# Performance work log

Measured on AMD Instinct MI355X. Metric: run time of the kernel, lower is better.

## Reference

```python
import jax, jax.numpy as jnp
import numpy as np

N, K, FC, FX, E = 16384, 16, 2, 32, 256


def _lin_init(key, fin, fout):
    kw, kb = jax.random.split(key)
    s = 1.0 / np.sqrt(fin)
    W = jax.random.uniform(kw, (fin, fout), jnp.float32, -s, s)
    b = jax.random.uniform(kb, (fout,), jnp.float32, -s, s)
    return W, b


def setup_inputs() -> dict:
    key = jax.random.key(0)
    ks = jax.random.split(key, 13)
    c = jax.random.uniform(ks[0], (N, FC), jnp.float32)
    x = jax.random.normal(ks[1], (N, FX), jnp.float32)
    W_coords, b_coords = _lin_init(ks[2], FC, E)
    W_attri, b_attri = _lin_init(ks[3], FX, E)
    W_g1, b_g1 = _lin_init(ks[4], FC, E)
    W_g2, b_g2 = _lin_init(ks[5], E, E)
    W_g3, b_g3 = _lin_init(ks[6], E, E)
    W_f1, b_f1 = _lin_init(ks[7], FX, E)
    W_f2, b_f2 = _lin_init(ks[8], E, E)
    W_f3, b_f3 = _lin_init(ks[9], E, E)
    W_d1, b_d1 = _lin_init(ks[10], 2 * E, 2 * E)
    W_d2, b_d2 = _lin_init(ks[11], 2 * E, 2)
    return dict(c=c, x=x,
                W_coords=W_coords, b_coords=b_coords,
                W_attri=W_attri, b_attri=b_attri,
                W_g1=W_g1, b_g1=b_g1, W_g2=W_g2, b_g2=b_g2, W_g3=W_g3, b_g3=b_g3,
                W_f1=W_f1, b_f1=b_f1, W_f2=W_f2, b_f2=b_f2, W_f3=W_f3, b_f3=b_f3,
                W_d1=W_d1, b_d1=b_d1, W_d2=W_d2, b_d2=b_d2)


def knn_edges(c, k):
    # PyG knn_graph (loop=False, flow='source_to_target'):
    # edge_index[0]=neighbor(src), edge_index[1]=node(dst).
    n = c.shape[0]
    sq = jnp.sum(c * c, axis=1)
    d2 = sq[:, None] + sq[None, :] - 2.0 * (c @ c.T)  # [N,N] squared dists
    d2 = d2.at[jnp.arange(n), jnp.arange(n)].set(jnp.inf)  # exclude self
    _, idx = jax.lax.top_k(-d2, k)  # [N,k] nearest neighbor indices
    src = idx.reshape(-1)
    dst = jnp.repeat(jnp.arange(n), k)
    return src, dst


def gcn_conv(h, src, dst, ew, W, b):
    # PyG GCNConv: linear -> add self-loops (weight 1) -> sym norm -> scatter-add -> +bias
    n = h.shape[0]
    hw = h @ W
    loop = jnp.arange(n)
    s = jnp.concatenate([src, loop])
    d = jnp.concatenate([dst, loop])
    w = jnp.concatenate([ew, jnp.ones((n,), h.dtype)])
    deg = jax.ops.segment_sum(w, d, num_segments=n)
    dinv = jnp.where(deg > 0, jax.lax.rsqrt(deg), 0.0)
    norm = dinv[s] * w * dinv[d]
    out = jax.ops.segment_sum(norm[:, None] * hw[s], d, num_segments=n)
    return out + b


def reference(c, x, W_coords, b_coords, W_attri, b_attri,
              W_g1, b_g1, W_g2, b_g2, W_g3, b_g3,
              W_f1, b_f1, W_f2, b_f2, W_f3, b_f3,
              W_d1, b_d1, W_d2, b_d2):
    src, dst = knn_edges(c, K)
    dist = jnp.linalg.norm(c[src] - c[dst], axis=1)
    ew = jnp.exp(-dist / 2.0)
    ew = jnp.where(ew > 10.0, 0.0, ew)  # faithful to source (never triggers)

    coords0 = c @ W_coords + b_coords
    attri0 = x @ W_attri + b_attri

    # eval mode: dropout is identity
    g1 = jax.nn.relu(gcn_conv(c, src, dst, ew, W_g1, b_g1))
    m1 = jax.nn.relu(x @ W_f1 + b_f1)
    g1 = coords0 + g1
    m1 = attri0 + m1

    g2 = jax.nn.relu(gcn_conv(g1, src, dst, ew, W_g2, b_g2))
    m2 = jax.nn.relu(m1 @ W_f2 + b_f2)
    g2 = g1 + g2
    m2 = m1 + m2

    g3 = jax.nn.relu(gcn_conv(g2, src, dst, ew, W_g3, b_g3))
    m3 = jax.nn.relu(m2 @ W_f3 + b_f3)
    g3 = g2 + g3
    m3 = m2 + m3

    combined = jnp.concatenate([g3, m3], axis=1)
    out = jax.nn.relu(combined @ W_d1 + b_d1) @ W_d2 + b_d2
    mean = out[:, 0]
    sigma = 0.2 + 0.8 * jax.nn.softplus(out[:, 1])
    return mean.reshape(-1, 1), sigma.reshape(-1, 1), g3, m3
```

## Files before the change

### kernel.cpp

```cpp
#include <hip/hip_runtime.h>
#include <math.h>

#define NPTS 16384
#define KNN 16
#define GRES 128
#define NCELL (GRES * GRES)
#define CAP 16

typedef unsigned long long ull;
typedef __attribute__((ext_vector_type(8))) short  bf16x8;
typedef __attribute__((ext_vector_type(4))) float  f32x4;

__device__ inline unsigned short f2bf(float f) {
    unsigned int u = __float_as_uint(f);
    u += 0x7fffu + ((u >> 16) & 1u);
    return (unsigned short)(u >> 16);
}
__device__ inline float bf2f(unsigned short u) {
    return __uint_as_float(((unsigned int)u) << 16);
}

__device__ inline void glds16(const void* g, void* l) {
    __builtin_amdgcn_global_load_lds((const __attribute__((address_space(1))) void*)g,
                                     (__attribute__((address_space(3))) void*)l, 16, 0, 0);
}

__global__ __launch_bounds__(256) void wprep_kernel(
    const float* __restrict__ W0, const float* __restrict__ W1,
    const float* __restrict__ W2, const float* __restrict__ W3,
    const float* __restrict__ W4,
    unsigned short* __restrict__ D0, unsigned short* __restrict__ D1,
    unsigned short* __restrict__ D2, unsigned short* __restrict__ D3,
    unsigned short* __restrict__ D4, int* __restrict__ cnt)
{
    const int z = blockIdx.z;
    if (z == 5) {
        const int i = (blockIdx.y * 16 + blockIdx.x) * 256 + threadIdx.x;
        if (i < NCELL) cnt[i] = 0;
        return;
    }
    const float* W; unsigned short* D; int K;
    if (z == 0) { W = W0; D = D0; K = 256; }
    else if (z == 1) { W = W1; D = D1; K = 256; }
    else if (z == 2) { W = W2; D = D2; K = 256; }
    else if (z == 3) { W = W3; D = D3; K = 256; }
    else { W = W4; D = D4; K = 512; }
    const int nt = K / 32;
    if (blockIdx.x >= nt || blockIdx.y >= nt) return;
    const int k0 = blockIdx.x * 32, n0 = blockIdx.y * 32;
    __shared__ float t[32][33];
    const int tr = threadIdx.x >> 5, tc = threadIdx.x & 31;
#pragma unroll
    for (int i = 0; i < 4; ++i)
        t[tr + i * 8][tc] = W[(size_t)(k0 + tr + i * 8) * K + n0 + tc];
    __syncthreads();
#pragma unroll
    for (int i = 0; i < 4; ++i)
        D[(size_t)(n0 + tr + i * 8) * K + k0 + tc] = f2bf(t[tc][tr + i * 8]);
}

__global__ __launch_bounds__(256) void count_scatter_kernel(const float2* __restrict__ c,
    int* __restrict__ cnt, float4* __restrict__ pts)
{
    const int i = blockIdx.x * 256 + threadIdx.x;
    float2 p = c[i];
    int cx = min(GRES - 1, max(0, (int)(p.x * GRES)));
    int cy = min(GRES - 1, max(0, (int)(p.y * GRES)));
    int cell = cy * GRES + cx;
    int slot = atomicAdd(&cnt[cell], 1);
    if (slot < CAP) {
        float4 v;
        v.x = p.x; v.y = p.y; v.z = __uint_as_float((unsigned int)i); v.w = 0.f;
        pts[cell * CAP + slot] = v;
    }
}

__global__ __launch_bounds__(256) void knn_query_kernel(const float2* __restrict__ c,
    const float4* __restrict__ pts, const int* __restrict__ cnt,
    int* __restrict__ nbr, float* __restrict__ ew, float* __restrict__ dinv)
{
    const int lane = threadIdx.x & 63;
    const int qidx = blockIdx.x * 4 + (threadIdx.x >> 6);
    const float2 qc = c[qidx];
    const float qx = qc.x, qy = qc.y;
    const int qcx = min(GRES - 1, max(0, (int)(qx * GRES)));
    const int qcy = min(GRES - 1, max(0, (int)(qy * GRES)));

    ull cur = ~0ULL;

    auto process = [&](int ccy, int ccx, bool valid) {
        int s0 = 0, len = 0;
        if (valid && ccy >= 0 && ccy < GRES && ccx >= 0 && ccx < GRES) {
            const int cell = ccy * GRES + ccx;
            s0 = cell * CAP;
            len = min(cnt[cell], CAP);
        }
        int pin = len;
#pragma unroll
        for (int off = 1; off < 64; off <<= 1) {
            int v = __shfl_up(pin, off, 64);
            pin += (lane >= off) ? v : 0;
        }
        const int T = __shfl(pin, 63, 64);
        const int pex = pin - len;
        for (int b = 0; b < T; b += 64) {
            const int ci = b + lane;
            const int cq = min(ci, T - 1);
            int lo = 0, hi = 63;
#pragma unroll
            for (int it = 0; it < 6; ++it) {
                const int mid = (lo + hi) >> 1;
                const int pm = __shfl(pin, mid, 64);
                if (pm > cq) hi = mid; else lo = mid + 1;
            }
            const int cs = __shfl(s0, hi, 64);
            const int cb = __shfl(pex, hi, 64);
            const int p  = cs + (cq - cb);
            const float4 pp = pts[p];
            const float dx = pp.x - qx, dy = pp.y - qy;
            const float d2 = fmaf(dx, dx, dy * dy);
            const int pidx = (int)__float_as_uint(pp.z);
            ull key = ~0ULL;
            if (ci < T && pidx != qidx)
                key = (((ull)__float_as_uint(d2)) << 32) | (ull)__float_as_uint(pp.z);
#pragma unroll
            for (int k = 2; k <= 64; k <<= 1) {
#pragma unroll
                for (int j = k >> 1; j > 0; j >>= 1) {
                    ull o = __shfl_xor(key, j, 64);
                    bool takeMin = (((lane & k) == 0) == ((lane & j) == 0));
                    ull mn = (o < key) ? o : key;
                    ull mx = (o > key) ? o : key;
                    key = takeMin ? mn : mx;
                }
            }
            ull rev = __shfl(key, (31 - lane) & 63, 64);
            ull val = (lane < 16) ? cur : ((lane < 32) ? rev : ~0ULL);
#pragma unroll
            for (int j = 16; j > 0; j >>= 1) {
                ull o = __shfl_xor(val, j, 64);
                ull mn = (o < val) ? o : val;
                ull mx = (o > val) ? o : val;
                val = ((lane & j) == 0) ? mn : mx;
            }
            cur = (lane < 16) ? val : ~0ULL;
        }
    };

    process(qcy - 3 + lane / 7, qcx - 3 + (lane % 7), lane < 49);

    int R = 3;
    const float h = 1.0f / GRES;
    while (true) {
        ull k15 = __shfl(cur, 15, 64);
        float dmax = __uint_as_float((unsigned int)(k15 >> 32));
        float rr = 0.999f * (float)R * h;
        if (dmax < rr * rr) break;
        if (R >= GRES) break;
        ++R;
        const int ncells = 8 * R;
        for (int cc = 0; cc < ncells; cc += 64) {
            const int i = cc + lane;
            int ccy = 0, ccx = 0;
            const bool valid = (i < ncells);
            if (valid) {
                const int side = 2 * R + 1;
                if (i < side)            { ccy = qcy - R; ccx = qcx - R + i; }
                else if (i < 2 * side)   { ccy = qcy + R; ccx = qcx - R + (i - side); }
                else {
                    const int j = i - 2 * side;
                    ccy = qcy - R + 1 + (j >> 1);
                    ccx = (j & 1) ? (qcx + R) : (qcx - R);
                }
            }
            process(ccy, ccx, valid);
        }
    }

    float w = 0.f; int nb = 0;
    if (lane < 16) {
        nb = (int)(cur & 0xffffffffu);
        float d2 = __uint_as_float((unsigned int)(cur >> 32));
        w = expf(-0.5f * sqrtf(d2));
    }
    float acc = w;
#pragma unroll
    for (int off = 1; off < 64; off <<= 1) acc += __shfl_xor(acc, off, 64);
    if (lane < 16) {
        nbr[qidx * KNN + lane] = nb;
        ew[qidx * KNN + lane]  = w;
    }
    if (lane == 0) dinv[qidx] = 1.0f / sqrtf(1.0f + acc);
}

__global__ __launch_bounds__(256) void init_fused_kernel(
    const float* __restrict__ x, const float2* __restrict__ c,
    const int* __restrict__ nbr, const float* __restrict__ ew, const float* __restrict__ dinv,
    const float* __restrict__ Wa, const float* __restrict__ ba,
    const float* __restrict__ Wf, const float* __restrict__ bf,
    const float* __restrict__ Wc, const float* __restrict__ bc,
    const float* __restrict__ Wg, const float* __restrict__ bg,
    float* __restrict__ m1f, unsigned short* __restrict__ m1b,
    float* __restrict__ g1f, unsigned short* __restrict__ g1b)
{
    __shared__ float smem[64 * 32];
    const int tid = threadIdx.x;
    if (blockIdx.x < 256) {
        const int i0 = blockIdx.x * 64;
#pragma unroll
        for (int it = 0; it < 8; ++it)
            smem[tid + it * 256] = x[(size_t)i0 * 32 + tid + it * 256];
        float wa[32], wf[32];
#pragma unroll
        for (int k = 0; k < 32; ++k) { wa[k] = Wa[k * 256 + tid]; wf[k] = Wf[k * 256 + tid]; }
        const float b0 = ba[tid], b1 = bf[tid];
        __syncthreads();
        for (int r = 0; r < 64; ++r) {
            float a0 = b0, a1 = b1;
#pragma unroll
            for (int k = 0; k < 32; ++k) {
                float xv = smem[r * 32 + k];
                a0 = fmaf(xv, wa[k], a0);
                a1 = fmaf(xv, wf[k], a1);
            }
            const float v = a0 + fmaxf(a1, 0.0f);
            m1f[(size_t)(i0 + r) * 256 + tid] = v;
            m1b[(size_t)(i0 + r) * 256 + tid] = f2bf(v);
        }
    } else {
        float (*su)[5] = (float(*)[5])smem;
        const int i0 = (blockIdx.x - 256) * 64;
        if (tid < 64) {
            const int i = i0 + tid;
            float ux = 0.f, uy = 0.f;
            for (int t = 0; t < KNN; ++t) {
                int nb = nbr[i * KNN + t];
                float w = ew[i * KNN + t] * dinv[nb];
                float2 cn = c[nb];
                ux = fmaf(w, cn.x, ux); uy = fmaf(w, cn.y, uy);
            }
            float di = dinv[i];
            float2 ci = c[i];
            ux = fmaf(di, ci.x, ux); uy = fmaf(di, ci.y, uy);
            su[tid][0] = ux; su[tid][1] = uy; su[tid][2] = ci.x; su[tid][3] = ci.y; su[tid][4] = di;
        }
        __syncthreads();
        const float wc0 = Wc[tid], wc1 = Wc[256 + tid];
        const float wg0 = Wg[tid], wg1 = Wg[256 + tid];
        const float bcj = bc[tid], bgj = bg[tid];
        for (int r = 0; r < 64; ++r) {
            float ux = su[r][0], uy = su[r][1], cx = su[r][2], cy = su[r][3], di = su[r][4];
            float coords0 = fmaf(cx, wc0, fmaf(cy, wc1, bcj));
            float pre = fmaf(di, fmaf(ux, wg0, uy * wg1), bgj);
            const float v = coords0 + fmaxf(pre, 0.0f);
            g1f[(size_t)(i0 + r) * 256 + tid] = v;
            g1b[(size_t)(i0 + r) * 256 + tid] = f2bf(v);
        }
    }
}

__global__ __launch_bounds__(256) void agg_kernel(const unsigned short* __restrict__ hw,
    const int* __restrict__ nbr, const float* __restrict__ ew, const float* __restrict__ dinv,
    const float* __restrict__ bias, const float* __restrict__ res,
    float* __restrict__ outf, unsigned short* __restrict__ outb)
{
    __shared__ int   sn[8][16];
    __shared__ float sw[8][16];
    __shared__ float sdi[8];
    const int tid = threadIdx.x;
    const int i0  = blockIdx.x * 8;
    if (tid < 128) {
        const int r = tid >> 4, t = tid & 15;
        const int i = i0 + r;
        const int nb = nbr[i * KNN + t];
        sn[r][t] = nb;
        sw[r][t] = ew[i * KNN + t] * dinv[nb];
        if (t == 0) sdi[r] = dinv[i];
    }
    __syncthreads();
    const int rl = tid >> 5;
    const int c0 = (tid & 31) * 8;
    const int i  = i0 + rl;
    const float di = sdi[rl];
    float acc[8];
    {
        const bf16x8 h = *(const bf16x8*)&hw[(size_t)i * 256 + c0];
#pragma unroll
        for (int e = 0; e < 8; ++e) acc[e] = di * bf2f((unsigned short)h[e]);
    }
#pragma unroll
    for (int t = 0; t < KNN; ++t) {
        const float w = sw[rl][t];
        const bf16x8 h = *(const bf16x8*)&hw[(size_t)sn[rl][t] * 256 + c0];
#pragma unroll
        for (int e = 0; e < 8; ++e) acc[e] = fmaf(w, bf2f((unsigned short)h[e]), acc[e]);
    }
    float bb[8], rv[8], vo[8];
    *(float4*)&bb[0] = *(const float4*)&bias[c0];
    *(float4*)&bb[4] = *(const float4*)&bias[c0 + 4];
    *(float4*)&rv[0] = *(const float4*)&res[(size_t)i * 256 + c0];
    *(float4*)&rv[4] = *(const float4*)&res[(size_t)i * 256 + c0 + 4];
    bf16x8 ob;
#pragma unroll
    for (int e = 0; e < 8; ++e) {
        float v = fmaf(di, acc[e], bb[e]);
        v = rv[e] + fmaxf(v, 0.0f);
        vo[e] = v;
        ob[e] = (short)f2bf(v);
    }
    *(float4*)&outf[(size_t)i * 256 + c0]     = *(const float4*)&vo[0];
    *(float4*)&outf[(size_t)i * 256 + c0 + 4] = *(const float4*)&vo[4];
    *(bf16x8*)&outb[(size_t)i * 256 + c0] = ob;
}

struct GemmOp {
    const unsigned short *A1, *A2; int ksplit;
    const unsigned short *Wt; int ncols, Kdim;
    const float *bias; const float *res;
    float *outf; unsigned short *outb;
    const float *Wd2; float *part;
    int flags;
};
__global__ __launch_bounds__(256) void gemm_bf16_kernel(GemmOp opA, GemmOp opB)
{
    const GemmOp op = (blockIdx.z == 0) ? opA : opB;
    __shared__ unsigned short As[2][128 * 64];
    __shared__ unsigned short Bs[2][128 * 64];
    const int tid = threadIdx.x;
    const int r0 = blockIdx.x * 128;
    const int c0 = blockIdx.y * 128;
    const int w  = tid >> 6;
    const int wr = w >> 1, wc = w & 1;
    const int l  = tid & 63;
    const int half = l >> 4, lc = l & 15;

    f32x4 acc[4][4];
#pragma unroll
    for (int mt = 0; mt < 4; ++mt)
#pragma unroll
        for (int nt = 0; nt < 4; ++nt) acc[mt][nt] = (f32x4){0.f, 0.f, 0.f, 0.f};

    auto stage = [&](int b, int k0) {
        const unsigned short* Asrc = (k0 < op.ksplit) ? (op.A1 + k0) : (op.A2 + (k0 - op.ksplit));
        const unsigned short* Bsrc = op.Wt + k0;
#pragma unroll
        for (int it = 0; it < 4; ++it) {
            const int g = tid + it * 256;
            const int r = g >> 3;
            const int s = (g & 7) ^ (r & 7);
            glds16(Asrc + (size_t)(r0 + r) * 256 + s * 8, &As[b][g * 8]);
        }
#pragma unroll
        for (int it = 0; it < 4; ++it) {
            const int g = tid + it * 256;
            const int r = g >> 3;
            const int s = (g & 7) ^ (r & 7);
            glds16(Bsrc + (size_t)(c0 + r) * op.Kdim + s * 8, &Bs[b][g * 8]);
        }
    };

    const int NT = op.Kdim >> 6;
    stage(0, 0);
    __syncthreads();
    int cur = 0;
    for (int t = 0; t < NT; ++t) {
        if (t + 1 < NT) stage(cur ^ 1, (t + 1) << 6);
#pragma unroll
        for (int ks = 0; ks < 2; ++ks) {
            bf16x8 af[4], bq[4];
#pragma unroll
            for (int mt = 0; mt < 4; ++mt) {
                const int rr = wr * 64 + mt * 16 + lc;
                af[mt] = *(const bf16x8*)&As[cur][rr * 64 + ((((ks << 2) + half) ^ (rr & 7)) << 3)];
            }
#pragma unroll
            for (int nt = 0; nt < 4; ++nt) {
                const int rr = wc * 64 + nt * 16 + lc;
                bq[nt] = *(const bf16x8*)&Bs[cur][rr * 64 + ((((ks << 2) + half) ^ (rr & 7)) << 3)];
            }
#pragma unroll
            for (int mt = 0; mt < 4; ++mt)
#pragma unroll
                for (int nt = 0; nt < 4; ++nt)
                    acc[mt][nt] = __builtin_amdgcn_mfma_f32_16x16x32_bf16(af[mt], bq[nt], acc[mt][nt], 0, 0, 0);
        }
        if (t + 1 < NT) { __syncthreads(); cur ^= 1; }
    }

    if (op.flags & 32) {
        float p0[4][4], p1[4][4];
#pragma unroll
        for (int mt = 0; mt < 4; ++mt)
#pragma unroll
            for (int r = 0; r < 4; ++r) { p0[mt][r] = 0.f; p1[mt][r] = 0.f; }
#pragma unroll
        for (int nt = 0; nt < 4; ++nt) {
            const int col = c0 + wc * 64 + nt * 16 + lc;
            const float bv = op.bias[col];
            const float w0 = op.Wd2[col * 2 + 0];
            const float w1 = op.Wd2[col * 2 + 1];
#pragma unroll
            for (int mt = 0; mt < 4; ++mt)
#pragma unroll
                for (int r = 0; r < 4; ++r) {
                    float v = fmaxf(acc[mt][nt][r] + bv, 0.f);
                    p0[mt][r] = fmaf(v, w0, p0[mt][r]);
                    p1[mt][r] = fmaf(v, w1, p1[mt][r]);
                }
        }
#pragma unroll
        for (int mt = 0; mt < 4; ++mt)
#pragma unroll
            for (int r = 0; r < 4; ++r) {
#pragma unroll
                for (int j = 1; j < 16; j <<= 1) {
                    p0[mt][r] += __shfl_xor(p0[mt][r], j, 64);
                    p1[mt][r] += __shfl_xor(p1[mt][r], j, 64);
                }
            }
        if (lc == 0) {
            float* part = op.part + ((size_t)blockIdx.y * 2 + wc) * NPTS * 2;
#pragma unroll
            for (int mt = 0; mt < 4; ++mt) {
                const int rowb = r0 + wr * 64 + mt * 16 + half * 4;
#pragma unroll
                for (int r = 0; r < 4; ++r) {
                    part[(size_t)(rowb + r) * 2 + 0] = p0[mt][r];
                    part[(size_t)(rowb + r) * 2 + 1] = p1[mt][r];
                }
            }
        }
        return;
    }
#pragma unroll
    for (int nt = 0; nt < 4; ++nt) {
        const int col = c0 + wc * 64 + nt * 16 + lc;
        const float bv = (op.flags & 1) ? op.bias[col] : 0.f;
#pragma unroll
        for (int mt = 0; mt < 4; ++mt) {
            const int rowb = r0 + wr * 64 + mt * 16 + half * 4;
#pragma unroll
            for (int r = 0; r < 4; ++r) {
                float v = acc[mt][nt][r] + bv;
                if (op.flags & 2) v = fmaxf(v, 0.f);
                if (op.flags & 4) v += op.res[(size_t)(rowb + r) * op.ncols + col];
                if (op.flags & 8)  op.outf[(size_t)(rowb + r) * op.ncols + col] = v;
                if (op.flags & 16) op.outb[(size_t)(rowb + r) * op.ncols + col] = f2bf(v);
            }
        }
    }
}

__global__ __launch_bounds__(256) void finish_kernel(const float* __restrict__ part,
    const float* __restrict__ b, float* __restrict__ mean, float* __restrict__ sigma)
{
    const int i = blockIdx.x * 256 + threadIdx.x;
    float a0 = 0.f, a1 = 0.f;
#pragma unroll
    for (int j = 0; j < 8; ++j) {
        a0 += part[(size_t)j * NPTS * 2 + 2 * i];
        a1 += part[(size_t)j * NPTS * 2 + 2 * i + 1];
    }
    mean[i] = a0 + b[0];
    float z = a1 + b[1];
    float sp = fmaxf(z, 0.f) + log1pf(expf(-fabsf(z)));
    sigma[i] = fmaf(0.8f, sp, 0.2f);
}

extern "C" void kernel_launch(void* const* d_in, const int* in_sizes, int n_in,
                              void* d_out, int out_size, void* d_ws, size_t ws_size,
                              hipStream_t stream)
{
    (void)in_sizes; (void)n_in; (void)out_size; (void)ws_size;
    const float* c   = (const float*)d_in[0];
    const float* x   = (const float*)d_in[1];
    const float* Wc  = (const float*)d_in[2];
    const float* bc  = (const float*)d_in[3];
    const float* Wa  = (const float*)d_in[4];
    const float* ba  = (const float*)d_in[5];
    const float* Wg1 = (const float*)d_in[6];
    const float* bg1 = (const float*)d_in[7];
    const float* Wg2 = (const float*)d_in[8];
    const float* bg2 = (const float*)d_in[9];
    const float* Wg3 = (const float*)d_in[10];
    const float* bg3 = (const float*)d_in[11];
    const float* Wf1 = (const float*)d_in[12];
    const float* bf1 = (const float*)d_in[13];
    const float* Wf2 = (const float*)d_in[14];
    const float* bf2 = (const float*)d_in[15];
    const float* Wf3 = (const float*)d_in[16];
    const float* bf3 = (const float*)d_in[17];
    const float* Wd1 = (const float*)d_in[18];
    const float* bd1 = (const float*)d_in[19];
    const float* Wd2 = (const float*)d_in[20];
    const float* bd2 = (const float*)d_in[21];

    float* out = (float*)d_out;
    const size_t N = NPTS;
    const size_t SLOT = N * 256;
    float* wsf  = (float*)d_ws;
    int*   nbr  = (int*)d_ws;
    float* ew   = wsf + N * 16;
    float* dinv = wsf + N * 32;
    float* s0   = wsf + N * 33;
    float* s1   = s0 + SLOT;
    float* s2   = s1 + SLOT;
    unsigned short* b0 = (unsigned short*)(s2 + SLOT);
    unsigned short* b1 = b0 + SLOT;
    unsigned short* b2 = b1 + SLOT;
    unsigned short* b3 = b2 + SLOT;
    unsigned short* wb = b3 + SLOT;
    unsigned short* bWg2 = wb;
    unsigned short* bWf2 = wb + 65536;
    unsigned short* bWg3 = wb + 131072;
    unsigned short* bWf3 = wb + 196608;
    unsigned short* bWd1 = wb + 262144;
    float* part = (float*)(wb + 262144 + 262144);

    float4* g_pts  = (float4*)s2;
    int* g_cnt     = (int*)(s2 + (size_t)NCELL * CAP * 4);

    float* o_mean  = out;
    float* o_sigma = out + N;
    float* o_g3    = out + 2 * N;
    float* o_m3    = out + 2 * N + N * 256;

    wprep_kernel<<<dim3(16, 16, 6), 256, 0, stream>>>(Wg2, Wf2, Wg3, Wf3, Wd1,
                                                      bWg2, bWf2, bWg3, bWf3, bWd1, g_cnt);
    count_scatter_kernel<<<NPTS / 256, 256, 0, stream>>>((const float2*)c, g_cnt, g_pts);
    knn_query_kernel<<<NPTS / 4, 256, 0, stream>>>((const float2*)c, g_pts, g_cnt, nbr, ew, dinv);
    init_fused_kernel<<<512, 256, 0, stream>>>(x, (const float2*)c, nbr, ew, dinv,
                                               Wa, ba, Wf1, bf1, Wc, bc, Wg1, bg1,
                                               s0, b0, s1, b1);

    GemmOp z{};
    GemmOp ohw2 = z; ohw2.A1 = b1; ohw2.A2 = b1; ohw2.ksplit = 256; ohw2.Wt = bWg2;
    ohw2.ncols = 256; ohw2.Kdim = 256; ohw2.outb = b2; ohw2.flags = 16;
    GemmOp om2 = z; om2.A1 = b0; om2.A2 = b0; om2.ksplit = 256; om2.Wt = bWf2;
    om2.ncols = 256; om2.Kdim = 256; om2.bias = bf2; om2.res = s0;
    om2.outf = s2; om2.outb = b3; om2.flags = 31;
    gemm_bf16_kernel<<<dim3(NPTS / 128, 2, 2), 256, 0, stream>>>(ohw2, om2);
    agg_kernel<<<NPTS / 8, 256, 0, stream>>>(b2, nbr, ew, dinv, bg2, s1, s1, b1);

    GemmOp ohw3 = z; ohw3.A1 = b1; ohw3.A2 = b1; ohw3.ksplit = 256; ohw3.Wt = bWg3;
    ohw3.ncols = 256; ohw3.Kdim = 256; ohw3.outb = b2; ohw3.flags = 16;
    GemmOp om3 = z; om3.A1 = b3; om3.A2 = b3; om3.ksplit = 256; om3.Wt = bWf3;
    om3.ncols = 256; om3.Kdim = 256; om3.bias = bf3; om3.res = s2;
    om3.outf = o_m3; om3.outb = b0; om3.flags = 31;
    gemm_bf16_kernel<<<dim3(NPTS / 128, 2, 2), 256, 0, stream>>>(ohw3, om3);
    agg_kernel<<<NPTS / 8, 256, 0, stream>>>(b2, nbr, ew, dinv, bg3, s1, o_g3, b1);

    GemmOp oh = z; oh.A1 = b1; oh.A2 = b0; oh.ksplit = 256; oh.Wt = bWd1;
    oh.ncols = 512; oh.Kdim = 512; oh.bias = bd1; oh.Wd2 = Wd2; oh.part = part;
    oh.flags = 32;
    gemm_bf16_kernel<<<dim3(NPTS / 128, 4, 1), 256, 0, stream>>>(oh, oh);
    finish_kernel<<<NPTS / 256, 256, 0, stream>>>(part, bd2, o_mean, o_sigma);
}
```

Baseline: 275.4 us.

## Fuse weight prep into kNN kernel and finish reduction into last GEMM

The weight transpose/bf16 conversion now runs as extra blocks of the kNN query kernel, and a tiny zero kernel handles the cell counters. The separate finish kernel is removed: each row-block of the final GEMM bumps an atomic counter, and the last of the four column blocks to finish reduces the partial sums and writes mean and sigma. This cuts launch count and small-kernel tail overhead. The cost is extra atomics and fences, plus reliance on cross-block ordering through the counter.

```diff
diff --git a/kernel.cpp b/kernel.cpp
--- a/kernel.cpp
+++ b/kernel.cpp
@@ -25,43 +25,15 @@
                                      (__attribute__((address_space(3))) void*)l, 16, 0, 0);
 }
 
-__global__ __launch_bounds__(256) void wprep_kernel(
-    const float* __restrict__ W0, const float* __restrict__ W1,
-    const float* __restrict__ W2, const float* __restrict__ W3,
-    const float* __restrict__ W4,
-    unsigned short* __restrict__ D0, unsigned short* __restrict__ D1,
-    unsigned short* __restrict__ D2, unsigned short* __restrict__ D3,
-    unsigned short* __restrict__ D4, int* __restrict__ cnt)
-{
-    const int z = blockIdx.z;
-    if (z == 5) {
-        const int i = (blockIdx.y * 16 + blockIdx.x) * 256 + threadIdx.x;
-        if (i < NCELL) cnt[i] = 0;
-        return;
-    }
-    const float* W; unsigned short* D; int K;
-    if (z == 0) { W = W0; D = D0; K = 256; }
-    else if (z == 1) { W = W1; D = D1; K = 256; }
-    else if (z == 2) { W = W2; D = D2; K = 256; }
-    else if (z == 3) { W = W3; D = D3; K = 256; }
-    else { W = W4; D = D4; K = 512; }
-    const int nt = K / 32;
-    if (blockIdx.x >= nt || blockIdx.y >= nt) return;
-    const int k0 = blockIdx.x * 32, n0 = blockIdx.y * 32;
-    __shared__ float t[32][33];
-    const int tr = threadIdx.x >> 5, tc = threadIdx.x & 31;
-#pragma unroll
-    for (int i = 0; i < 4; ++i)
-        t[tr + i * 8][tc] = W[(size_t)(k0 + tr + i * 8) * K + n0 + tc];
-    __syncthreads();
-#pragma unroll
-    for (int i = 0; i < 4; ++i)
-        D[(size_t)(n0 + tr + i * 8) * K + k0 + tc] = f2bf(t[tc][tr + i * 8]);
+__global__ __launch_bounds__(256) void zero_cnt_kernel(int* __restrict__ cnt)
+{
+    cnt[blockIdx.x * 256 + threadIdx.x] = 0;
 }
 
 __global__ __launch_bounds__(256) void count_scatter_kernel(const float2* __restrict__ c,
-    int* __restrict__ cnt, float4* __restrict__ pts)
-{
+    int* __restrict__ cnt, float4* __restrict__ pts, int* __restrict__ hctr)
+{
+    if (blockIdx.x == 0 && threadIdx.x < 128) hctr[threadIdx.x] = 0;
     const int i = blockIdx.x * 256 + threadIdx.x;
     float2 p = c[i];
     int cx = min(GRES - 1, max(0, (int)(p.x * GRES)));
@@ -75,12 +47,45 @@
     }
 }
 
-__global__ __launch_bounds__(256) void knn_query_kernel(const float2* __restrict__ c,
+__global__ __launch_bounds__(256) void knn_wprep_kernel(const float2* __restrict__ c,
     const float4* __restrict__ pts, const int* __restrict__ cnt,
-    int* __restrict__ nbr, float* __restrict__ ew, float* __restrict__ dinv)
-{
+    int* __restrict__ nbr, float* __restrict__ ew, float* __restrict__ dinv,
+    const float* __restrict__ W0, const float* __restrict__ W1,
+    const float* __restrict__ W2, const float* __restrict__ W3,
+    const float* __restrict__ W4,
+    unsigned short* __restrict__ D0, unsigned short* __restrict__ D1,
+    unsigned short* __restrict__ D2, unsigned short* __restrict__ D3,
+    unsigned short* __restrict__ D4)
+{
+    if (blockIdx.x < 512) {
+        const int wb = blockIdx.x;
+        const float* W; unsigned short* D; int K, bx, by;
+        if (wb < 256) {
+            const int z = wb >> 6, r = wb & 63;
+            bx = r & 7; by = r >> 3; K = 256;
+            if (z == 0) { W = W0; D = D0; }
+            else if (z == 1) { W = W1; D = D1; }
+            else if (z == 2) { W = W2; D = D2; }
+            else { W = W3; D = D3; }
+        } else {
+            const int r = wb - 256;
+            bx = r & 15; by = r >> 4; K = 512; W = W4; D = D4;
+        }
+        const int k0 = bx * 32, n0 = by * 32;
+        __shared__ float t[32][33];
+        const int tr = threadIdx.x >> 5, tc = threadIdx.x & 31;
+#pragma unroll
+        for (int i = 0; i < 4; ++i)
+            t[tr + i * 8][tc] = W[(size_t)(k0 + tr + i * 8) * K + n0 + tc];
+        __syncthreads();
+#pragma unroll
+        for (int i = 0; i < 4; ++i)
+            D[(size_t)(n0 + tr + i * 8) * K + k0 + tc] = f2bf(t[tc][tr + i * 8]);
+        return;
+    }
+
     const int lane = threadIdx.x & 63;
-    const int qidx = blockIdx.x * 4 + (threadIdx.x >> 6);
+    const int qidx = (blockIdx.x - 512) * 4 + (threadIdx.x >> 6);
     const float2 qc = c[qidx];
     const float qx = qc.x, qy = qc.y;
     const int qcx = min(GRES - 1, max(0, (int)(qx * GRES)));
@@ -319,6 +324,7 @@
     const float *bias; const float *res;
     float *outf; unsigned short *outb;
     const float *Wd2; float *part;
+    int *hctr; float *meanp; float *sigmap; const float *bd2;
     int flags;
 };
 __global__ __launch_bounds__(256) void gemm_bf16_kernel(GemmOp opA, GemmOp opB)
@@ -326,6 +332,7 @@
     const GemmOp op = (blockIdx.z == 0) ? opA : opB;
     __shared__ unsigned short As[2][128 * 64];
     __shared__ unsigned short Bs[2][128 * 64];
+    __shared__ int sdone;
     const int tid = threadIdx.x;
     const int r0 = blockIdx.x * 128;
     const int c0 = blockIdx.y * 128;
@@ -430,6 +437,29 @@
                 }
             }
         }
+        __syncthreads();
+        if (tid == 0) {
+            __threadfence();
+            sdone = __hip_atomic_fetch_add(op.hctr + blockIdx.x, 1,
+                                           __ATOMIC_ACQ_REL, __HIP_MEMORY_SCOPE_AGENT);
+        }
+        __syncthreads();
+        if (sdone == 3) {
+            __threadfence();
+            const int row = blockIdx.x * 128 + (tid >> 1);
+            const int j = tid & 1;
+            float a = 0.f;
+#pragma unroll
+            for (int s = 0; s < 8; ++s)
+                a += op.part[(size_t)s * NPTS * 2 + (size_t)row * 2 + j];
+            if (j == 0) {
+                op.meanp[row] = a + op.bd2[0];
+            } else {
+                float z = a + op.bd2[1];
+                float sp = fmaxf(z, 0.f) + log1pf(expf(-fabsf(z)));
+                op.sigmap[row] = fmaf(0.8f, sp, 0.2f);
+            }
+        }
         return;
     }
 #pragma unroll
@@ -449,22 +479,6 @@
             }
         }
     }
-}
-
-__global__ __launch_bounds__(256) void finish_kernel(const float* __restrict__ part,
-    const float* __restrict__ b, float* __restrict__ mean, float* __restrict__ sigma)
-{
-    const int i = blockIdx.x * 256 + threadIdx.x;
-    float a0 = 0.f, a1 = 0.f;
-#pragma unroll
-    for (int j = 0; j < 8; ++j) {
-        a0 += part[(size_t)j * NPTS * 2 + 2 * i];
-        a1 += part[(size_t)j * NPTS * 2 + 2 * i + 1];
-    }
-    mean[i] = a0 + b[0];
-    float z = a1 + b[1];
-    float sp = fmaxf(z, 0.f) + log1pf(expf(-fabsf(z)));
-    sigma[i] = fmaf(0.8f, sp, 0.2f);
 }
 
 extern "C" void kernel_launch(void* const* d_in, const int* in_sizes, int n_in,
@@ -516,6 +530,7 @@
     unsigned short* bWf3 = wb + 196608;
     unsigned short* bWd1 = wb + 262144;
     float* part = (float*)(wb + 262144 + 262144);
+    int* hctr   = (int*)(part + 8 * N * 2);
 
     float4* g_pts  = (float4*)s2;
     int* g_cnt     = (int*)(s2 + (size_t)NCELL * CAP * 4);
@@ -525,10 +540,12 @@
     float* o_g3    = out + 2 * N;
     float* o_m3    = out + 2 * N + N * 256;
 
-    wprep_kernel<<<dim3(16, 16, 6), 256, 0, stream>>>(Wg2, Wf2, Wg3, Wf3, Wd1,
-                                                      bWg2, bWf2, bWg3, bWf3, bWd1, g_cnt);
-    count_scatter_kernel<<<NPTS / 256, 256, 0, stream>>>((const float2*)c, g_cnt, g_pts);
-    knn_query_kernel<<<NPTS / 4, 256, 0, stream>>>((const float2*)c, g_pts, g_cnt, nbr, ew, dinv);
+    zero_cnt_kernel<<<NCELL / 256, 256, 0, stream>>>(g_cnt);
+    count_scatter_kernel<<<NPTS / 256, 256, 0, stream>>>((const float2*)c, g_cnt, g_pts, hctr);
+    knn_wprep_kernel<<<512 + NPTS / 4, 256, 0, stream>>>((const float2*)c, g_pts, g_cnt,
+                                                         nbr, ew, dinv,
+                                                         Wg2, Wf2, Wg3, Wf3, Wd1,
+                                                         bWg2, bWf2, bWg3, bWf3, bWd1);
     init_fused_kernel<<<512, 256, 0, stream>>>(x, (const float2*)c, nbr, ew, dinv,
                                                Wa, ba, Wf1, bf1, Wc, bc, Wg1, bg1,
                                                s0, b0, s1, b1);
@@ -552,7 +569,7 @@
 
     GemmOp oh = z; oh.A1 = b1; oh.A2 = b0; oh.ksplit = 256; oh.Wt = bWd1;
     oh.ncols = 512; oh.Kdim = 512; oh.bias = bd1; oh.Wd2 = Wd2; oh.part = part;
+    oh.hctr = hctr; oh.meanp = o_mean; oh.sigmap = o_sigma; oh.bd2 = bd2;
     oh.flags = 32;
     gemm_bf16_kernel<<<dim3(NPTS / 128, 4, 1), 256, 0, stream>>>(oh, oh);
-    finish_kernel<<<NPTS / 256, 256, 0, stream>>>(part, bd2, o_mean, o_sigma);
-}
+}
```

Result: slower. 300.9 us (+9.3%).
